# Optimization experiments

Measured on AMD Instinct MI355X. Metric: run time of the kernel, lower is better.

## Reference

```python
import jax, jax.numpy as jnp
import numpy as np
from jax import lax

SCORE_T = 0.05
NMS_T = 0.5
MAXDET = 300


def batch_iou(b1, b2):
    # b1: [K,4], b2: [K,4] -> [K,K]
    lt = jnp.maximum(b1[:, None, :2], b2[None, :, :2])
    rb = jnp.minimum(b1[:, None, 2:], b2[None, :, 2:])
    inter = jnp.clip(rb - lt, 0.0, None).prod(-1)
    a1 = (b1[:, 2:] - b1[:, :2]).prod(-1)
    a2 = (b2[:, 2:] - b2[:, :2]).prod(-1)
    union = a1[:, None] + a2[None, :] - inter
    return inter / jnp.clip(union, 1e-7, None)


def nms_class(boxes, cls_scores):
    # boxes: [N,4], cls_scores: [N]. Mirrors: score>thresh filter, top-k MAXDET
    # candidates, greedy NMS in descending score order.
    s = jnp.where(cls_scores > SCORE_T, cls_scores, -jnp.inf)
    top_s, idx = lax.top_k(s, MAXDET)          # sorted desc, [K]
    b = jnp.take(boxes, idx, axis=0)            # [K,4]
    v = jnp.isfinite(top_s)                     # passed score threshold
    iou = batch_iou(b, b)                       # [K,K]

    def body(kept, i):
        # keep i iff valid and no already-kept box has IoU >= NMS_T with it
        suppressed = jnp.any(jnp.where(kept, iou[i], 0.0) >= NMS_T)
        return kept.at[i].set(v[i] & ~suppressed), None

    kept, _ = lax.scan(body, jnp.zeros(MAXDET, dtype=bool), jnp.arange(MAXDET))
    return top_s, idx, kept


def per_image(boxes, cls):
    # boxes: [N,4], cls: [N,C]
    C = cls.shape[1]
    top_s, idx, kept = jax.vmap(nms_class, in_axes=(None, 1))(boxes, cls)  # [C,K]
    scores_flat = jnp.where(kept, top_s, -jnp.inf).reshape(-1)  # [C*K]
    idx_flat = idx.reshape(-1)
    labels_flat = jnp.repeat(jnp.arange(C), MAXDET)
    fs, fi = lax.top_k(scores_flat, MAXDET)     # global top-k across classes
    valid = jnp.isfinite(fs)
    box_idx = idx_flat[fi]
    out_boxes = jnp.where(valid[:, None], jnp.take(boxes, box_idx, axis=0), -1.0)
    out_scores = jnp.where(valid, fs, -1.0)
    out_labels = jnp.where(valid, labels_flat[fi], -1).astype(jnp.int32)
    return out_boxes, out_scores, out_labels


def setup_inputs() -> dict:
    key = jax.random.key(0)
    k1, k2, k3 = jax.random.split(key, 3)
    B, N, C = 8, 100000, 80
    centers = jax.random.uniform(k1, (B, N, 2), dtype=jnp.float32) * 1024.0
    wh = jax.random.uniform(k2, (B, N, 2), dtype=jnp.float32) * 96.0 + 4.0
    boxes = jnp.concatenate([centers - wh / 2, centers + wh / 2], axis=-1)
    classification = jax.random.uniform(k3, (B, N, C), dtype=jnp.float32)
    return {"boxes": boxes, "classification": classification}


def reference(boxes, classification):
    # Returns (Boxes [B,MAXDET,4], Scores [B,MAXDET], Labels [B,MAXDET] int32),
    # padded with -1 where fewer than MAXDET detections survive.
    return jax.vmap(per_image)(boxes, classification)
```

## Files before the change

kernel.cpp:

```cpp
#include <hip/hip_runtime.h>

#define BIMG 8
#define NBOX 100000
#define NCLS 80
#define KDET 300
#define CAP  2048
#define CAPC 20
#define TPUSH 0.984375f
#define SCORE_T 0.05f
#define NELEM 8000000
#define NQ    2000000

typedef unsigned long long u64;
typedef unsigned u32;

#define OFF_PUSHCNT 0u
#define ZERO_BYTES  2560u
#define OFF_BUF     4096u
#define OFF_KCNT    (4096u + 10485760u)
#define OFF_KSC     (OFF_KCNT + 2560u)
#define OFF_KIDX    (OFF_KSC + 768000u)

static __device__ __forceinline__ u64 mk_key(float sc, u32 n) {
  return ((u64)__float_as_uint(sc) << 32) | (u32)(~n);
}

static __device__ __forceinline__ void radix_step(const u32* hist, int nbins,
                                                  int width, u32* sk, u64* spfx,
                                                  u32* stot) {
  if (threadIdx.x < 64) {
    const int lane = threadIdx.x;
    const int chunk = nbins >> 6;
    u32 psum = 0;
    for (int i = 0; i < chunk; ++i) psum += hist[lane * chunk + i];
    u32 suf = psum;
#pragma unroll
    for (int off = 1; off < 64; off <<= 1) {
      u32 o = __shfl_down(suf, off);
      if (lane + off < 64) suf += o;
    }
    if (lane == 0) *stot = suf;
    u32 k = *sk;
    u64 bal = __ballot(suf >= k);
    if (bal != 0ull) {
      int L = 63 - __clzll((long long)bal);
      if (lane == L) {
        u32 krem = k - (suf - psum);
        int bi = (L + 1) * chunk - 1;
        u32 acc = 0;
        for (;;) {
          acc += hist[bi];
          if (acc >= krem || bi == L * chunk) break;
          --bi;
        }
        *spfx = (*spfx << width) | (u32)bi;
        *sk = krem - (acc - hist[bi]);
      }
    }
  }
}

__constant__ int RSH[6] = {53, 42, 31, 20, 9, 0};
__constant__ int RWD[6] = {11, 11, 11, 11, 11, 9};

static __device__ __forceinline__ void pushone(int c, float sc, u32 n, int b,
                                               u32* lcnt, u64* stage,
                                               u32* pushcnt, u64* buf) {
  u64 key = mk_key(sc, n);
  u32 slot = atomicAdd(&lcnt[c], 1u);
  if (slot < CAPC) {
    stage[c * CAPC + slot] = key;
  } else {
    u32 g = atomicAdd(&pushcnt[b * NCLS + c], 1u);
    if (g < CAP) buf[(size_t)(b * NCLS + c) * CAP + g] = key;
  }
}

__global__ __launch_bounds__(256) void histK(const float* __restrict__ cls,
                                             u32* __restrict__ pushcnt,
                                             u64* __restrict__ buf) {
  __shared__ u32 lcnt[NCLS];
  __shared__ u32 sbase[NCLS];
  __shared__ u64 stage[NCLS * CAPC];

  const int t = threadIdx.x;
  const int b = blockIdx.y;
  for (int i = t; i < NCLS; i += 256) lcnt[i] = 0;
  __syncthreads();

  const float4* base4 = (const float4*)(cls + (size_t)b * NELEM);
  const int start = blockIdx.x * 8192;

#define PROCQ(u) do { \
    float mx = fmaxf(fmaxf(v##u.x, v##u.y), fmaxf(v##u.z, v##u.w)); \
    if (mx >= TPUSH) { \
      const int e0 = q##u * 4; \
      const int c0 = e0 % NCLS; \
      const u32 n = (u32)(e0 / NCLS); \
      if (v##u.x >= TPUSH) pushone(c0 + 0, v##u.x, n, b, lcnt, stage, pushcnt, buf); \
      if (v##u.y >= TPUSH) pushone(c0 + 1, v##u.y, n, b, lcnt, stage, pushcnt, buf); \
      if (v##u.z >= TPUSH) pushone(c0 + 2, v##u.z, n, b, lcnt, stage, pushcnt, buf); \
      if (v##u.w >= TPUSH) pushone(c0 + 3, v##u.w, n, b, lcnt, stage, pushcnt, buf); \
    } } while (0)

  if (start + 8192 <= NQ) {
    for (int it = 0; it < 4; ++it) {
      const int qb = start + it * 2048 + t;
#define LOADF(u) const int q##u = qb + (u) * 256; const float4 v##u = base4[q##u]
      LOADF(0); LOADF(1); LOADF(2); LOADF(3);
      LOADF(4); LOADF(5); LOADF(6); LOADF(7);
#undef LOADF
      PROCQ(0); PROCQ(1); PROCQ(2); PROCQ(3);
      PROCQ(4); PROCQ(5); PROCQ(6); PROCQ(7);
    }
  } else {
    for (int it = 0; it < 4; ++it) {
      const int qb = start + it * 2048 + t;
#define LOADC(u) const int q##u = qb + (u) * 256; \
  const float4 v##u = (q##u < NQ) ? base4[q##u] : make_float4(0.f, 0.f, 0.f, 0.f)
      LOADC(0); LOADC(1); LOADC(2); LOADC(3);
      LOADC(4); LOADC(5); LOADC(6); LOADC(7);
#undef LOADC
      PROCQ(0); PROCQ(1); PROCQ(2); PROCQ(3);
      PROCQ(4); PROCQ(5); PROCQ(6); PROCQ(7);
    }
  }
#undef PROCQ
  __syncthreads();

  if (t < NCLS) {
    u32 cnt = min(lcnt[t], (u32)CAPC);
    sbase[t] = cnt ? atomicAdd(&pushcnt[b * NCLS + t], cnt) : 0u;
  }
  __syncthreads();
  for (int idx = t; idx < NCLS * CAPC; idx += 256) {
    const int c = idx / CAPC;
    const int k = idx - c * CAPC;
    if ((u32)k < min(lcnt[c], (u32)CAPC)) {
      u32 s = sbase[c] + (u32)k;
      if (s < CAP) buf[(size_t)(b * NCLS + c) * CAP + s] = stage[idx];
    }
  }
}

__global__ __launch_bounds__(512) void nmsK(const float* __restrict__ boxes,
                                            const float* __restrict__ cls,
                                            const u32* __restrict__ pushcnt,
                                            u64* __restrict__ buf,
                                            u32* __restrict__ keptCnt,
                                            float* __restrict__ keptScore,
                                            u32* __restrict__ keptIdx) {
  __shared__ float bx[KDET][4];
  __shared__ float scl[KDET];
  __shared__ u32 nn_[KDET];
  __shared__ u64 msk[KDET][5];
  __shared__ u64 tk[512];
  __shared__ u64 keptw[5];
  __shared__ u64 spfx;
  __shared__ u32 sk, stot, stcnt;
  __shared__ u32 sfpfx, sfk, sfab, sfeq, sfmode, sfbcnt;

  const int t = threadIdx.x;
  const int bc = blockIdx.x;
  const int b = bc / NCLS;
  u64* bufp = buf + (size_t)bc * CAP;
  u32* hist = (u32*)&msk[0][0];

  if (t == 0) { spfx = 0ull; sk = KDET; stcnt = 0u; sfmode = 0u; sfbcnt = 0u; }

  u32 realcnt = pushcnt[bc];
  const bool dofb = !(realcnt >= (u32)KDET && realcnt <= (u32)CAP);
  if (dofb) {
    const int c = bc % NCLS;
    const float* col = cls + (size_t)b * NELEM + c;
    for (int r = 0; r < 3; ++r) {
      const int shift = (r == 0) ? 21 : (r == 1) ? 10 : 0;
      const int nbins = (r == 2) ? 1024 : 2048;
      for (int i = t; i < nbins; i += 512) hist[i] = 0;
      __syncthreads();
      for (int n = t; n < NBOX; n += 512) {
        float sc = col[(size_t)n * NCLS];
        if (sc > SCORE_T) {
          u32 u = __float_as_uint(sc);
          bool ok = (r == 0) || (r == 1 ? ((u >> 21) == (sfpfx >> 21))
                                        : ((u >> 10) == (sfpfx >> 10)));
          if (ok) atomicAdd(&hist[(u >> shift) & (u32)(nbins - 1)], 1u);
        }
      }
      __syncthreads();
      if (t == 0) {
        if (r == 0) {
          u32 s = 0;
          for (int i = 0; i < nbins; ++i) s += hist[i];
          if (s < KDET) sfmode = 1u;
        }
        if (sfmode == 0u) {
          u32 kk2 = (r == 0) ? (u32)KDET : sfk;
          u32 acc = 0;
          int bi = nbins - 1;
          for (; bi >= 0; --bi) {
            if (acc + hist[bi] >= kk2) break;
            acc += hist[bi];
          }
          sfk = kk2 - acc;
          sfpfx = ((r == 0) ? 0u : sfpfx) | ((u32)bi << shift);
          if (r == 2) { sfeq = hist[bi]; sfab = KDET - sfk; }
        }
      }
      __syncthreads();
      if (sfmode == 1u) break;
    }

    if (sfmode == 1u) {
      for (int n = t; n < NBOX; n += 512) {
        float sc = col[(size_t)n * NCLS];
        if (sc > SCORE_T) {
          u32 g = atomicAdd(&sfbcnt, 1u);
          if (g < CAP) bufp[g] = mk_key(sc, (u32)n);
        }
      }
    } else {
      const u32 ustar = sfpfx;
      const u32 m = sfab, e = sfeq;
      if (m + e <= CAP) {
        for (int n = t; n < NBOX; n += 512) {
          float sc = col[(size_t)n * NCLS];
          if (sc > SCORE_T && __float_as_uint(sc) >= ustar) {
            u32 g = atomicAdd(&sfbcnt, 1u);
            if (g < CAP) bufp[g] = mk_key(sc, (u32)n);
          }
        }
      } else {
        for (int n = t; n < NBOX; n += 512) {
          float sc = col[(size_t)n * NCLS];
          if (sc > SCORE_T && __float_as_uint(sc) > ustar) {
            u32 g = atomicAdd(&sfbcnt, 1u);
            if (g < CAP) bufp[g] = mk_key(sc, (u32)n);
          }
        }
        __syncthreads();
        if (t == 0) {
          u32 room = CAP - m, got = 0;
          for (int n = 0; n < NBOX && got < room; ++n) {
            float sc = col[(size_t)n * NCLS];
            if (sc > SCORE_T && __float_as_uint(sc) == ustar) {
              u32 g = atomicAdd(&sfbcnt, 1u);
              if (g < CAP) bufp[g] = mk_key(sc, (u32)n);
              ++got;
            }
          }
        }
      }
    }
    __threadfence_block();
    __syncthreads();
    realcnt = sfbcnt;
  }
  const int cnt = min((int)realcnt, CAP);

  u64 kk[4];
#pragma unroll
  for (int u = 0; u < 4; ++u) {
    int i = t + u * 512;
    u64 v = 0ull;
    if (i < cnt)
      v = dofb ? *((volatile const u64*)(bufp + i)) : bufp[i];
    kk[u] = v;
  }

  const bool normal = (cnt > KDET);
  if (normal) {
    for (int p = 0; p < 6; ++p) {
      const int nb = (p == 5) ? 512 : 2048;
      for (int i = t; i < nb; i += 512) hist[i] = 0;
      __syncthreads();
      const u64 pfx = spfx;
#pragma unroll
      for (int u = 0; u < 4; ++u) {
        u64 key = kk[u];
        if (!key) continue;
        if (p > 0 && (key >> RSH[p - 1]) != pfx) continue;
        atomicAdd(&hist[(u32)(key >> RSH[p]) & (u32)(nb - 1)], 1u);
      }
      __syncthreads();
      radix_step(hist, nb, RWD[p], &sk, &spfx, &stot);
      __syncthreads();
    }
  } else {
    __syncthreads();
  }
  const u64 thr = normal ? spfx : 1ull;

  tk[t] = 0ull;
  __syncthreads();
#pragma unroll
  for (int u = 0; u < 4; ++u) {
    u64 key = kk[u];
    if (key >= thr && key != 0ull) {
      u32 pos = atomicAdd(&stcnt, 1u);
      if (pos < 512) tk[pos] = key;
    }
  }
  __syncthreads();

  u64 a = tk[t];
#pragma unroll
  for (int k2 = 2; k2 <= 64; k2 <<= 1) {
#pragma unroll
    for (int j = k2 >> 1; j > 0; j >>= 1) {
      u64 c2 = __shfl_xor(a, j);
      bool takeMax = (((t & k2) == 0) == ((t & j) == 0));
      u64 mx = (a > c2) ? a : c2;
      u64 mn = (a > c2) ? c2 : a;
      a = takeMax ? mx : mn;
    }
  }
#pragma unroll
  for (int k2 = 128; k2 <= 512; k2 <<= 1) {
    for (int j = k2 >> 1; j >= 64; j >>= 1) {
      tk[t] = a;
      __syncthreads();
      u64 c2 = tk[t ^ j];
      bool takeMax = (((t & k2) == 0) == ((t & j) == 0));
      u64 mx = (a > c2) ? a : c2;
      u64 mn = (a > c2) ? c2 : a;
      a = takeMax ? mx : mn;
      __syncthreads();
    }
#pragma unroll
    for (int j = 32; j > 0; j >>= 1) {
      u64 c2 = __shfl_xor(a, j);
      bool takeMax = (((t & k2) == 0) == ((t & j) == 0));
      u64 mx = (a > c2) ? a : c2;
      u64 mn = (a > c2) ? c2 : a;
      a = takeMax ? mx : mn;
    }
  }
  tk[t] = a;
  __syncthreads();

  const int M = min((int)stcnt, KDET);
  for (int i = t; i < M; i += 512) {
    u64 key = tk[i];
    u32 n = ~(u32)key;
    scl[i] = __uint_as_float((u32)(key >> 32));
    nn_[i] = n;
    const float4 bv = *(const float4*)(boxes + ((size_t)b * NBOX + n) * 4);
    bx[i][0] = bv.x; bx[i][1] = bv.y; bx[i][2] = bv.z; bx[i][3] = bv.w;
  }
  __syncthreads();

  for (int i = t; i < M; i += 512) {
    float x1 = bx[i][0], y1 = bx[i][1], x2 = bx[i][2], y2 = bx[i][3];
    float a1 = (x2 - x1) * (y2 - y1);
    u64 m0 = 0, m1 = 0, m2 = 0, m3 = 0, m4 = 0;
    for (int j = 0; j < i; ++j) {
      float lx = fmaxf(x1, bx[j][0]);
      float ly = fmaxf(y1, bx[j][1]);
      float rx = fminf(x2, bx[j][2]);
      float ry = fminf(y2, bx[j][3]);
      float iw = fmaxf(rx - lx, 0.0f), ih = fmaxf(ry - ly, 0.0f);
      float inter = iw * ih;
      float a2 = (bx[j][2] - bx[j][0]) * (bx[j][3] - bx[j][1]);
      float uni = fmaxf(a1 + a2 - inter, 1e-7f);
      float iou = inter / uni;
      if (iou >= 0.5f) {
        u64 bit = 1ull << (j & 63);
        switch (j >> 6) {
          case 0: m0 |= bit; break;
          case 1: m1 |= bit; break;
          case 2: m2 |= bit; break;
          case 3: m3 |= bit; break;
          default: m4 |= bit; break;
        }
      }
    }
    msk[i][0] = m0; msk[i][1] = m1; msk[i][2] = m2; msk[i][3] = m3; msk[i][4] = m4;
  }
  __syncthreads();

  if (t < 64) {
    u64 kwv[5];
#pragma unroll
    for (int w = 0; w < 5; ++w) {
      const int i = w * 64 + t;
      bool pb = (i < M);
      u64 mown = 0ull;
      if (pb) {
#pragma unroll
        for (int w2 = 0; w2 < 5; ++w2)
          if (w2 < w && (msk[i][w2] & kwv[w2])) pb = false;
        mown = msk[i][w];
      }
      u64 kv = 0ull;
      for (;;) {
        u64 bal = __ballot(pb && ((mown & kv) == 0ull));
        if (!bal) break;
        int p = __ffsll((unsigned long long)bal) - 1;
        kv |= 1ull << p;
        if (t == p) pb = false;
      }
      kwv[w] = kv;
      if (t == 0) keptw[w] = kv;
    }
  }
  __syncthreads();

  for (int i = t; i < M; i += 512) {
    if ((keptw[i >> 6] >> (i & 63)) & 1ull) {
      int rank = 0;
      for (int w = 0; w < (i >> 6); ++w) rank += __popcll(keptw[w]);
      rank += __popcll(keptw[i >> 6] & ((1ull << (i & 63)) - 1ull));
      keptScore[(size_t)bc * KDET + rank] = scl[i];
      keptIdx[(size_t)bc * KDET + rank] = nn_[i];
    }
  }
  if (t == 0) {
    int tot = 0;
    for (int w = 0; w < 5; ++w) tot += __popcll(keptw[w]);
    keptCnt[bc] = (u32)tot;
  }
}

#define MSLOT 24
__global__ __launch_bounds__(1024) void mergeK(const float* __restrict__ boxes,
                                               const u32* __restrict__ keptCnt,
                                               const float* __restrict__ keptScore,
                                               const u32* __restrict__ keptIdx,
                                               float* __restrict__ out) {
  __shared__ u32 hist[4 * 2048];
  __shared__ int scnt[NCLS];
  __shared__ u64 tk[512];
  __shared__ u64 spfx, sthr;
  __shared__ u32 sk, stot, smode, stcnt;

  const int t = threadIdx.x;
  const int b = blockIdx.x;
  if (t < NCLS) scnt[t] = min((int)keptCnt[b * NCLS + t], KDET);
  if (t == 0) { spfx = 0ull; sk = KDET; smode = 0u; stcnt = 0u; }
  __syncthreads();

  u64 kk[MSLOT];
  const float* ksc = keptScore + (size_t)b * NCLS * KDET;
#pragma unroll
  for (int u = 0; u < MSLOT; ++u) {
    int idx = t + u * 1024;
    u64 key = 0ull;
    if (idx < NCLS * KDET) {
      int c = idx / KDET, r = idx - c * KDET;
      if (r < scnt[c])
        key = ((u64)__float_as_uint(ksc[idx]) << 32) | (u32)(~(u32)idx);
    }
    kk[u] = key;
  }

  for (int p = 0; p < 6; ++p) {
    const int nb = (p == 5) ? 512 : 2048;
    for (int i = t; i < 4 * 2048; i += 1024) hist[i] = 0;
    __syncthreads();
    u32* hp = hist + ((t >> 8) & 3) * 2048;
    const u64 pfx = spfx;
#pragma unroll
    for (int u = 0; u < MSLOT; ++u) {
      u64 key = kk[u];
      if (!key) continue;
      if (p > 0 && (key >> RSH[p - 1]) != pfx) continue;
      atomicAdd(&hp[(u32)(key >> RSH[p]) & (u32)(nb - 1)], 1u);
    }
    __syncthreads();
    for (int i = t; i < nb; i += 1024)
      hist[i] = hist[i] + hist[2048 + i] + hist[4096 + i] + hist[6144 + i];
    __syncthreads();
    radix_step(hist, nb, RWD[p], &sk, &spfx, &stot);
    __syncthreads();
    if (p == 0) {
      if (t == 0 && stot <= KDET) smode = 1u;
      __syncthreads();
      if (smode) break;
    }
  }
  if (t == 0) sthr = smode ? 1ull : spfx;
  if (t < 512) tk[t] = 0ull;
  __syncthreads();

  const u64 thr = sthr;
#pragma unroll
  for (int u = 0; u < MSLOT; ++u) {
    u64 key = kk[u];
    if (key >= thr && key != 0ull) {
      u32 pos = atomicAdd(&stcnt, 1u);
      if (pos < 512) tk[pos] = key;
    }
  }
  __syncthreads();

  for (int k2 = 2; k2 <= 512; k2 <<= 1) {
    for (int j = k2 >> 1; j > 0; j >>= 1) {
      if (t < 512) {
        int i = t, ixj = i ^ j;
        if (ixj > i) {
          u64 a = tk[i], c2 = tk[ixj];
          bool up = ((i & k2) == 0);
          if (up ? (a < c2) : (a > c2)) { tk[i] = c2; tk[ixj] = a; }
        }
      }
      __syncthreads();
    }
  }

  if (t < KDET) {
    float* ob = out + ((size_t)b * KDET + t) * 4;
    float* os = out + (size_t)BIMG * KDET * 4;
    float* ol = os + (size_t)BIMG * KDET;
    u64 key = tk[t];
    if (key == 0ull) {
      *(float4*)ob = make_float4(-1.f, -1.f, -1.f, -1.f);
      os[(size_t)b * KDET + t] = -1.f;
      ol[(size_t)b * KDET + t] = -1.f;
    } else {
      u32 fi = ~(u32)key;
      int c = fi / KDET, r = fi - c * KDET;
      u32 n = keptIdx[((size_t)b * NCLS + c) * KDET + r];
      *(float4*)ob = *(const float4*)(boxes + ((size_t)b * NBOX + n) * 4);
      os[(size_t)b * KDET + t] = __uint_as_float((u32)(key >> 32));
      ol[(size_t)b * KDET + t] = (float)c;
    }
  }
}

extern "C" void kernel_launch(void* const* d_in, const int* in_sizes, int n_in,
                              void* d_out, int out_size, void* d_ws, size_t ws_size,
                              hipStream_t stream) {
  const float* boxes = (const float*)d_in[0];
  const float* cls = (const float*)d_in[1];
  float* out = (float*)d_out;
  char* ws = (char*)d_ws;

  u32* pushcnt = (u32*)(ws + OFF_PUSHCNT);
  u64* buf = (u64*)(ws + OFF_BUF);
  u32* keptCnt = (u32*)(ws + OFF_KCNT);
  float* keptScore = (float*)(ws + OFF_KSC);
  u32* keptIdx = (u32*)(ws + OFF_KIDX);

  (void)hipMemsetAsync(ws + OFF_PUSHCNT, 0, ZERO_BYTES, stream);

  histK<<<dim3(245, BIMG), 256, 0, stream>>>(cls, pushcnt, buf);
  nmsK<<<BIMG * NCLS, 512, 0, stream>>>(boxes, cls, pushcnt, buf, keptCnt,
                                        keptScore, keptIdx);
  mergeK<<<BIMG, 1024, 0, stream>>>(boxes, keptCnt, keptScore, keptIdx, out);
}
```

Baseline: 513.0 us.

## Fuse merge into NMS kernel via last-block-per-image counter and skip trivial radix passes

Removes the separate merge kernel. The last NMS block to finish for each image, found through an atomic per-image counter, now does the cross-class top-k merge with 512 threads and a shuffle-based bitonic sort. Radix-select passes are skipped when the AND and OR of all keys show a digit is the same for every key. The push threshold and per-block staging capacity also change. This saves a kernel launch and some histogram passes, but the merge now runs on fewer threads inside the tail block and adds threadfence and atomic serialisation.

```diff
diff --git a/kernel.cpp b/kernel.cpp
--- a/kernel.cpp
+++ b/kernel.cpp
@@ -5,8 +5,8 @@
 #define NCLS 80
 #define KDET 300
 #define CAP  2048
-#define CAPC 20
-#define TPUSH 0.984375f
+#define CAPC 12
+#define TPUSH 0.9921875f
 #define SCORE_T 0.05f
 #define NELEM 8000000
 #define NQ    2000000
@@ -15,7 +15,8 @@
 typedef unsigned u32;
 
 #define OFF_PUSHCNT 0u
-#define ZERO_BYTES  2560u
+#define OFF_IMGDONE 2560u
+#define ZERO_BYTES  2592u
 #define OFF_BUF     4096u
 #define OFF_KCNT    (4096u + 10485760u)
 #define OFF_KSC     (OFF_KCNT + 2560u)
@@ -63,6 +64,44 @@
 __constant__ int RSH[6] = {53, 42, 31, 20, 9, 0};
 __constant__ int RWD[6] = {11, 11, 11, 11, 11, 9};
 
+static __device__ __forceinline__ void bitonic512(u64* tk, int t) {
+  u64 a = tk[t];
+#pragma unroll
+  for (int k2 = 2; k2 <= 64; k2 <<= 1) {
+#pragma unroll
+    for (int j = k2 >> 1; j > 0; j >>= 1) {
+      u64 c2 = __shfl_xor(a, j);
+      bool takeMax = (((t & k2) == 0) == ((t & j) == 0));
+      u64 mx = (a > c2) ? a : c2;
+      u64 mn = (a > c2) ? c2 : a;
+      a = takeMax ? mx : mn;
+    }
+  }
+#pragma unroll
+  for (int k2 = 128; k2 <= 512; k2 <<= 1) {
+    for (int j = k2 >> 1; j >= 64; j >>= 1) {
+      tk[t] = a;
+      __syncthreads();
+      u64 c2 = tk[t ^ j];
+      bool takeMax = (((t & k2) == 0) == ((t & j) == 0));
+      u64 mx = (a > c2) ? a : c2;
+      u64 mn = (a > c2) ? c2 : a;
+      a = takeMax ? mx : mn;
+      __syncthreads();
+    }
+#pragma unroll
+    for (int j = 32; j > 0; j >>= 1) {
+      u64 c2 = __shfl_xor(a, j);
+      bool takeMax = (((t & k2) == 0) == ((t & j) == 0));
+      u64 mx = (a > c2) ? a : c2;
+      u64 mn = (a > c2) ? c2 : a;
+      a = takeMax ? mx : mn;
+    }
+  }
+  tk[t] = a;
+  __syncthreads();
+}
+
 static __device__ __forceinline__ void pushone(int c, float sc, u32 n, int b,
                                                u32* lcnt, u64* stage,
                                                u32* pushcnt, u64* buf) {
@@ -149,7 +188,9 @@
                                             u64* __restrict__ buf,
                                             u32* __restrict__ keptCnt,
                                             float* __restrict__ keptScore,
-                                            u32* __restrict__ keptIdx) {
+                                            u32* __restrict__ keptIdx,
+                                            u32* __restrict__ imgDone,
+                                            float* __restrict__ out) {
   __shared__ float bx[KDET][4];
   __shared__ float scl[KDET];
   __shared__ u32 nn_[KDET];
@@ -157,7 +198,9 @@
   __shared__ u64 tk[512];
   __shared__ u64 keptw[5];
   __shared__ u64 spfx;
-  __shared__ u32 sk, stot, stcnt;
+  __shared__ u64 sand, sor;
+  __shared__ u32 sk, stot, stcnt, smtot, smerge;
+  __shared__ int msc[NCLS];
   __shared__ u32 sfpfx, sfk, sfab, sfeq, sfmode, sfbcnt;
 
   const int t = threadIdx.x;
@@ -270,8 +313,37 @@
 
   const bool normal = (cnt > KDET);
   if (normal) {
+    if (t == 0) { sand = ~0ull; sor = 0ull; }
+    __syncthreads();
+    {
+      u64 ka = ~0ull, ko = 0ull;
+#pragma unroll
+      for (int u = 0; u < 4; ++u) {
+        u64 key = kk[u];
+        if (key) { ka &= key; ko |= key; }
+      }
+#pragma unroll
+      for (int off = 32; off > 0; off >>= 1) {
+        ka &= __shfl_xor(ka, off);
+        ko |= __shfl_xor(ko, off);
+      }
+      if ((t & 63) == 0) {
+        atomicAnd((unsigned long long*)&sand, (unsigned long long)ka);
+        atomicOr((unsigned long long*)&sor, (unsigned long long)ko);
+      }
+    }
+    __syncthreads();
+    const u64 kand = sand, kor = sor;
     for (int p = 0; p < 6; ++p) {
       const int nb = (p == 5) ? 512 : 2048;
+      const u32 mask = (u32)(nb - 1);
+      const u32 ba = (u32)(kand >> RSH[p]) & mask;
+      const u32 bo = (u32)(kor >> RSH[p]) & mask;
+      if (ba == bo) {
+        if (t == 0) spfx = (spfx << RWD[p]) | (u64)ba;
+        __syncthreads();
+        continue;
+      }
       for (int i = t; i < nb; i += 512) hist[i] = 0;
       __syncthreads();
       const u64 pfx = spfx;
@@ -280,7 +352,7 @@
         u64 key = kk[u];
         if (!key) continue;
         if (p > 0 && (key >> RSH[p - 1]) != pfx) continue;
-        atomicAdd(&hist[(u32)(key >> RSH[p]) & (u32)(nb - 1)], 1u);
+        atomicAdd(&hist[(u32)(key >> RSH[p]) & mask], 1u);
       }
       __syncthreads();
       radix_step(hist, nb, RWD[p], &sk, &spfx, &stot);
@@ -303,41 +375,7 @@
   }
   __syncthreads();
 
-  u64 a = tk[t];
-#pragma unroll
-  for (int k2 = 2; k2 <= 64; k2 <<= 1) {
-#pragma unroll
-    for (int j = k2 >> 1; j > 0; j >>= 1) {
-      u64 c2 = __shfl_xor(a, j);
-      bool takeMax = (((t & k2) == 0) == ((t & j) == 0));
-      u64 mx = (a > c2) ? a : c2;
-      u64 mn = (a > c2) ? c2 : a;
-      a = takeMax ? mx : mn;
-    }
-  }
-#pragma unroll
-  for (int k2 = 128; k2 <= 512; k2 <<= 1) {
-    for (int j = k2 >> 1; j >= 64; j >>= 1) {
-      tk[t] = a;
-      __syncthreads();
-      u64 c2 = tk[t ^ j];
-      bool takeMax = (((t & k2) == 0) == ((t & j) == 0));
-      u64 mx = (a > c2) ? a : c2;
-      u64 mn = (a > c2) ? c2 : a;
-      a = takeMax ? mx : mn;
-      __syncthreads();
-    }
-#pragma unroll
-    for (int j = 32; j > 0; j >>= 1) {
-      u64 c2 = __shfl_xor(a, j);
-      bool takeMax = (((t & k2) == 0) == ((t & j) == 0));
-      u64 mx = (a > c2) ? a : c2;
-      u64 mn = (a > c2) ? c2 : a;
-      a = takeMax ? mx : mn;
-    }
-  }
-  tk[t] = a;
-  __syncthreads();
+  bitonic512(tk, t);
 
   const int M = min((int)stcnt, KDET);
   for (int i = t; i < M; i += 512) {
@@ -420,93 +458,91 @@
     for (int w = 0; w < 5; ++w) tot += __popcll(keptw[w]);
     keptCnt[bc] = (u32)tot;
   }
-}
-
-#define MSLOT 24
-__global__ __launch_bounds__(1024) void mergeK(const float* __restrict__ boxes,
-                                               const u32* __restrict__ keptCnt,
-                                               const float* __restrict__ keptScore,
-                                               const u32* __restrict__ keptIdx,
-                                               float* __restrict__ out) {
-  __shared__ u32 hist[4 * 2048];
-  __shared__ int scnt[NCLS];
-  __shared__ u64 tk[512];
-  __shared__ u64 spfx, sthr;
-  __shared__ u32 sk, stot, smode, stcnt;
-
-  const int t = threadIdx.x;
-  const int b = blockIdx.x;
-  if (t < NCLS) scnt[t] = min((int)keptCnt[b * NCLS + t], KDET);
-  if (t == 0) { spfx = 0ull; sk = KDET; smode = 0u; stcnt = 0u; }
-  __syncthreads();
-
-  u64 kk[MSLOT];
+  __syncthreads();
+
+  if (t == 0) {
+    __threadfence();
+    u32 done = atomicAdd(&imgDone[b], 1u);
+    smerge = (done == NCLS - 1) ? 1u : 0u;
+  }
+  __syncthreads();
+  if (!smerge) return;
+  __threadfence();
+
+  if (t == 0) { spfx = 0ull; sk = KDET; stcnt = 0u; smtot = 0u; sand = ~0ull; sor = 0ull; }
+  if (t < NCLS) msc[t] = min((int)keptCnt[b * NCLS + t], KDET);
+  __syncthreads();
+
   const float* ksc = keptScore + (size_t)b * NCLS * KDET;
-#pragma unroll
-  for (int u = 0; u < MSLOT; ++u) {
-    int idx = t + u * 1024;
-    u64 key = 0ull;
-    if (idx < NCLS * KDET) {
-      int c = idx / KDET, r = idx - c * KDET;
-      if (r < scnt[c])
-        key = ((u64)__float_as_uint(ksc[idx]) << 32) | (u32)(~(u32)idx);
-    }
-    kk[u] = key;
-  }
-
-  for (int p = 0; p < 6; ++p) {
-    const int nb = (p == 5) ? 512 : 2048;
-    for (int i = t; i < 4 * 2048; i += 1024) hist[i] = 0;
-    __syncthreads();
-    u32* hp = hist + ((t >> 8) & 3) * 2048;
-    const u64 pfx = spfx;
-#pragma unroll
-    for (int u = 0; u < MSLOT; ++u) {
-      u64 key = kk[u];
-      if (!key) continue;
-      if (p > 0 && (key >> RSH[p - 1]) != pfx) continue;
-      atomicAdd(&hp[(u32)(key >> RSH[p]) & (u32)(nb - 1)], 1u);
-    }
-    __syncthreads();
-    for (int i = t; i < nb; i += 1024)
-      hist[i] = hist[i] + hist[2048 + i] + hist[4096 + i] + hist[6144 + i];
-    __syncthreads();
-    radix_step(hist, nb, RWD[p], &sk, &spfx, &stot);
-    __syncthreads();
-    if (p == 0) {
-      if (t == 0 && stot <= KDET) smode = 1u;
-      __syncthreads();
-      if (smode) break;
-    }
-  }
-  if (t == 0) sthr = smode ? 1ull : spfx;
-  if (t < 512) tk[t] = 0ull;
-  __syncthreads();
-
-  const u64 thr = sthr;
-#pragma unroll
-  for (int u = 0; u < MSLOT; ++u) {
-    u64 key = kk[u];
-    if (key >= thr && key != 0ull) {
+#define MKEY(idx, key) do { \
+    int c_ = (idx) / KDET, r_ = (idx) - c_ * KDET; \
+    key = (r_ < msc[c_]) ? ((u64)__float_as_uint(ksc[idx]) << 32) | (u32)(~(u32)(idx)) \
+                         : 0ull; \
+  } while (0)
+
+  {
+    u64 ka = ~0ull, ko = 0ull;
+    u32 mycnt = 0;
+    for (int idx = t; idx < NCLS * KDET; idx += 512) {
+      u64 key; MKEY(idx, key);
+      if (key) { ka &= key; ko |= key; ++mycnt; }
+    }
+#pragma unroll
+    for (int off = 32; off > 0; off >>= 1) {
+      ka &= __shfl_xor(ka, off);
+      ko |= __shfl_xor(ko, off);
+      mycnt += __shfl_xor(mycnt, off);
+    }
+    if ((t & 63) == 0) {
+      atomicAnd((unsigned long long*)&sand, (unsigned long long)ka);
+      atomicOr((unsigned long long*)&sor, (unsigned long long)ko);
+      atomicAdd(&smtot, mycnt);
+    }
+  }
+  __syncthreads();
+
+  const bool mnormal = ((int)smtot > KDET);
+  if (mnormal) {
+    const u64 kand = sand, kor = sor;
+    for (int p = 0; p < 6; ++p) {
+      const int nb = (p == 5) ? 512 : 2048;
+      const u32 mask = (u32)(nb - 1);
+      const u32 ba = (u32)(kand >> RSH[p]) & mask;
+      const u32 bo = (u32)(kor >> RSH[p]) & mask;
+      if (ba == bo) {
+        if (t == 0) spfx = (spfx << RWD[p]) | (u64)ba;
+        __syncthreads();
+        continue;
+      }
+      for (int i = t; i < nb; i += 512) hist[i] = 0;
+      __syncthreads();
+      const u64 pfx = spfx;
+      for (int idx = t; idx < NCLS * KDET; idx += 512) {
+        u64 key; MKEY(idx, key);
+        if (!key) continue;
+        if (p > 0 && (key >> RSH[p - 1]) != pfx) continue;
+        atomicAdd(&hist[(u32)(key >> RSH[p]) & mask], 1u);
+      }
+      __syncthreads();
+      radix_step(hist, nb, RWD[p], &sk, &spfx, &stot);
+      __syncthreads();
+    }
+  }
+  const u64 mthr = mnormal ? spfx : 1ull;
+
+  tk[t] = 0ull;
+  __syncthreads();
+  for (int idx = t; idx < NCLS * KDET; idx += 512) {
+    u64 key; MKEY(idx, key);
+    if (key >= mthr && key != 0ull) {
       u32 pos = atomicAdd(&stcnt, 1u);
       if (pos < 512) tk[pos] = key;
     }
   }
   __syncthreads();
-
-  for (int k2 = 2; k2 <= 512; k2 <<= 1) {
-    for (int j = k2 >> 1; j > 0; j >>= 1) {
-      if (t < 512) {
-        int i = t, ixj = i ^ j;
-        if (ixj > i) {
-          u64 a = tk[i], c2 = tk[ixj];
-          bool up = ((i & k2) == 0);
-          if (up ? (a < c2) : (a > c2)) { tk[i] = c2; tk[ixj] = a; }
-        }
-      }
-      __syncthreads();
-    }
-  }
+#undef MKEY
+
+  bitonic512(tk, t);
 
   if (t < KDET) {
     float* ob = out + ((size_t)b * KDET + t) * 4;
@@ -537,6 +573,7 @@
   char* ws = (char*)d_ws;
 
   u32* pushcnt = (u32*)(ws + OFF_PUSHCNT);
+  u32* imgDone = (u32*)(ws + OFF_IMGDONE);
   u64* buf = (u64*)(ws + OFF_BUF);
   u32* keptCnt = (u32*)(ws + OFF_KCNT);
   float* keptScore = (float*)(ws + OFF_KSC);
@@ -546,6 +583,5 @@
 
   histK<<<dim3(245, BIMG), 256, 0, stream>>>(cls, pushcnt, buf);
   nmsK<<<BIMG * NCLS, 512, 0, stream>>>(boxes, cls, pushcnt, buf, keptCnt,
-                                        keptScore, keptIdx);
-  mergeK<<<BIMG, 1024, 0, stream>>>(boxes, keptCnt, keptScore, keptIdx, out);
-}
+                                        keptScore, keptIdx, imgDone, out);
+}
```

Result: slower. 543.9 us (+6.0%).
